# Optimization experiments

Measured on AMD Instinct MI355X. Metric: run time of the kernel, lower is better.

## Reference

```python
import math
import jax, jax.numpy as jnp
import numpy as np

K_KDE = 50
K_RIPS = 16
SCALE = 30.0
DESTNUM = 10
THRESHOLD = 1.0  # hardcoded in topograd_loss
N, D = 8192, 64


def _knn(x, k):
    """Brute-force k-NN with squared L2 distances (faiss IndexFlatL2 semantics,
    self included as nearest neighbour). Returns (sq_dists[N,k], idxs[N,k]),
    neighbours sorted by increasing distance."""
    sq = jnp.sum(x * x, axis=1)
    d = sq[:, None] + sq[None, :] - 2.0 * (x @ x.T)  # [N,N]
    neg, idx = jax.lax.top_k(-d, k)
    return -neg, idx


def _cluster(density, rips_idxs, threshold):
    """Union-find re-implementation of the numba `cluster` routine.
    Iterates points from high density (index N-1) to low; each point joins the
    entry of its highest-index upward neighbour; other upward neighbours'
    entries are merged if their persistence is below threshold, and every
    cross-entry comparison emits a persistence pair (entry_idx, ref_idx).
    Returns the raw pers_pairs array (without the [-1,-1] sentinel rows)."""
    n = density.shape[0]
    parent = np.arange(n)
    name = np.arange(n)  # name[root] = entry id (a point index)

    def find(i):
        root = i
        while parent[root] != root:
            root = parent[root]
        while parent[i] != root:  # path compression
            parent[i], i = root, parent[i]
        return root

    pairs = []
    for i in range(n - 2, -1, -1):
        nbr = rips_idxs[i]
        us = nbr[nbr > i]  # upward (denser, already-processed) neighbours
        if us.size == 0:
            continue  # point i forms its own singleton entry
        e_up = name[find(int(us.max()))]
        parent[find(i)] = find(e_up)  # append i to entry e_up
        for j in us:
            ei = name[find(int(j))]
            if ei != e_up:
                pairs.append((ei, i))
                if density[ei] - density[i] < threshold:
                    parent[find(ei)] = find(e_up)  # merge entry ei into e_up
    return np.asarray(pairs, dtype=np.int64).reshape(-1, 2)


def _pd_pairs(pairs, n):
    """For each unique entry id in pairs[:,0], keep (entry_id, max ref idx)."""
    maxref = np.full(n, -1, dtype=np.int64)
    np.maximum.at(maxref, pairs[:, 0], pairs[:, 1])
    uniq = np.unique(pairs[:, 0])
    return np.stack([uniq, maxref[uniq]], axis=1)


def setup_inputs() -> dict:
    key = jax.random.key(0)
    x = jax.random.normal(key, (N, D), dtype=jnp.float32)
    return {"x": x}


def reference(x):
    # --- KNN kernel density estimate (differentiable) ---
    vals, _ = _knn(x, K_KDE)
    res = jnp.sum(jnp.exp(-vals / SCALE), axis=1) / (K_KDE * SCALE)
    dens = res / jnp.max(res)
    # --- sort by ascending density ---
    sorted_idxs = jnp.argsort(dens)
    dens_s = dens[sorted_idxs]
    x_s = x[sorted_idxs]
    # --- delta-Rips graph on sorted points ---
    _, rips_idxs = _knn(x_s, K_RIPS)
    # --- persistence clustering (non-differentiable, host) ---
    pairs = _cluster(np.asarray(dens_s), np.asarray(rips_idxs), THRESHOLD)
    pd = jnp.asarray(_pd_pairs(pairs, x.shape[0]))  # [P,2] int64
    # --- topological loss ---
    oripd = dens_s[pd]  # [P,2] (birth, death) densities
    sidx = jnp.argsort(oripd[:, 0] - oripd[:, 1])  # ascending persistence
    changepairs = pd[sidx[:-DESTNUM]]
    nochangepairs = pd[sidx[-DESTNUM:-1]]
    dest = jax.lax.stop_gradient(oripd[sidx[-1]])  # torch.as_tensor detaches
    pd11 = dens_s[changepairs]
    weakdist = jnp.sum(pd11[:, 0] - pd11[:, 1]) / math.sqrt(2.0)
    strongdist = jnp.sum(jnp.linalg.norm(dens_s[nochangepairs] - dest, axis=1))
    return weakdist + strongdist
```

## Files before the change

### kernel.cpp

```cpp
#include <hip/hip_runtime.h>
#include <stdint.h>

#define NN 8192
#define DD 64

__global__ __launch_bounds__(256) void k_pre(const float* __restrict__ x, float* __restrict__ xT,
                                             float* __restrict__ sq, int do_tr){
  __shared__ float tile[64*65];
  const int tid = threadIdx.x;
  const int b = blockIdx.x;
  for (int k = 0; k < 4; ++k){
    const int idx4 = tid + k*256;
    const float4 v = ((const float4*)(x + (size_t)b*4096))[idx4];
    const int row = idx4 >> 4, d0 = (idx4 & 15) * 4;
    tile[row*65 + d0 + 0] = v.x;
    tile[row*65 + d0 + 1] = v.y;
    tile[row*65 + d0 + 2] = v.z;
    tile[row*65 + d0 + 3] = v.w;
  }
  __syncthreads();
  if (do_tr){
    const int jj = tid & 15;
    const int dq = tid >> 4;
    for (int k = 0; k < 4; ++k){
      const int d = dq + 16*k;
      float4 o;
      o.x = tile[(jj*4+0)*65 + d];
      o.y = tile[(jj*4+1)*65 + d];
      o.z = tile[(jj*4+2)*65 + d];
      o.w = tile[(jj*4+3)*65 + d];
      ((float4*)xT)[(size_t)d*2048 + b*16 + jj] = o;
    }
  }
  if (tid < 64){
    float acc = 0.f;
    const float* rp = tile + tid*65;
    for (int d = 0; d < 64; ++d) acc = fmaf(rp[d], rp[d], acc);
    sq[b*64 + tid] = acc;
  }
}

template<bool XT>
__device__ __forceinline__ void dists_1024(const float* __restrict__ x, const float* __restrict__ xT,
                                           const float* __restrict__ xi, int jbase, int tid,
                                           float acc[8][4]){
#pragma unroll
  for (int r = 0; r < 8; ++r)
#pragma unroll
    for (int q = 0; q < 4; ++q) acc[r][q] = 0.f;
  const int j0 = jbase + tid*4;
  for (int dq = 0; dq < 16; ++dq){
    float4 vj[4];
    if (XT){
#pragma unroll
      for (int s = 0; s < 4; ++s)
        vj[s] = ((const float4*)xT)[(size_t)(dq*4+s)*2048 + (j0 >> 2)];
    } else {
#pragma unroll
      for (int s = 0; s < 4; ++s){
        const int d = dq*4 + s;
        vj[s].x = x[(size_t)(j0+0)*64 + d];
        vj[s].y = x[(size_t)(j0+1)*64 + d];
        vj[s].z = x[(size_t)(j0+2)*64 + d];
        vj[s].w = x[(size_t)(j0+3)*64 + d];
      }
    }
#pragma unroll
    for (int r = 0; r < 8; ++r){
      const float4 wv = ((const float4*)(xi + r*64))[dq];
      acc[r][0] = fmaf(vj[0].x, wv.x, acc[r][0]);
      acc[r][1] = fmaf(vj[0].y, wv.x, acc[r][1]);
      acc[r][2] = fmaf(vj[0].z, wv.x, acc[r][2]);
      acc[r][3] = fmaf(vj[0].w, wv.x, acc[r][3]);
      acc[r][0] = fmaf(vj[1].x, wv.y, acc[r][0]);
      acc[r][1] = fmaf(vj[1].y, wv.y, acc[r][1]);
      acc[r][2] = fmaf(vj[1].z, wv.y, acc[r][2]);
      acc[r][3] = fmaf(vj[1].w, wv.y, acc[r][3]);
      acc[r][0] = fmaf(vj[2].x, wv.z, acc[r][0]);
      acc[r][1] = fmaf(vj[2].y, wv.z, acc[r][1]);
      acc[r][2] = fmaf(vj[2].z, wv.z, acc[r][2]);
      acc[r][3] = fmaf(vj[2].w, wv.z, acc[r][3]);
      acc[r][0] = fmaf(vj[3].x, wv.w, acc[r][0]);
      acc[r][1] = fmaf(vj[3].y, wv.w, acc[r][1]);
      acc[r][2] = fmaf(vj[3].z, wv.w, acc[r][2]);
      acc[r][3] = fmaf(vj[3].w, wv.w, acc[r][3]);
    }
  }
}

template<bool XT>
__global__ __launch_bounds__(256) void k_cand(const float* __restrict__ x, const float* __restrict__ xT,
                                              const float* __restrict__ sq,
                                              float* __restrict__ res, unsigned short* __restrict__ nn16){
  __shared__ float xi[8*64];
  __shared__ float sqi_s[8];
  __shared__ float tubs[8];
  __shared__ __align__(16) unsigned long long cand[8*512];
  __shared__ unsigned ccnt[8];
  float* samp = (float*)cand;
  const int tid = threadIdx.x;
  const int i0 = blockIdx.x * 8;
  for (int t = tid; t < 8*64; t += 256) xi[t] = x[(size_t)i0*64 + t];
  if (tid < 8){ sqi_s[tid] = sq[i0+tid]; ccnt[tid] = 0u; }
  __syncthreads();
  float sqir[8];
#pragma unroll
  for (int r = 0; r < 8; ++r) sqir[r] = sqi_s[r];

  const int w0 = (blockIdx.x * 1024) & 8191;
  {
    float acc[8][4];
    dists_1024<XT>(x, xT, xi, w0, tid, acc);
    float sqj[4];
#pragma unroll
    for (int q = 0; q < 4; ++q) sqj[q] = sq[w0 + tid*4 + q];
#pragma unroll
    for (int r = 0; r < 8; ++r)
#pragma unroll
      for (int q = 0; q < 4; ++q)
        samp[r*1024 + tid*4 + q] = (sqir[r] + sqj[q]) - 2.f*acc[r][q];
  }
  __syncthreads();
  {
    const int wv = tid >> 6, lane = tid & 63;
    for (int rr = 0; rr < 2; ++rr){
      const int r = wv + rr*4;
      float v[16];
#pragma unroll
      for (int k2 = 0; k2 < 16; ++k2) v[k2] = samp[r*1024 + lane + 64*k2];
      unsigned lo = 0u, hi = 0x7F800001u;
      while (hi - lo > 1u){
        const unsigned mid = (lo + hi) >> 1;
        const float pf = __uint_as_float(mid);
        int c = 0;
#pragma unroll
        for (int k2 = 0; k2 < 16; ++k2) c += (v[k2] < pf) ? 1 : 0;
#pragma unroll
        for (int off = 32; off; off >>= 1) c += __shfl_xor(c, off);
        if (c >= 32) hi = mid; else lo = mid;
      }
      if (lane == 0) tubs[r] = __uint_as_float(hi);
    }
  }
  __syncthreads();
  float tubr[8];
#pragma unroll
  for (int r = 0; r < 8; ++r) tubr[r] = tubs[r];
  for (int t = tid; t < 8*512; t += 256) cand[t] = ~0ULL;
  __syncthreads();

  for (int pass = 0; pass < 8; ++pass){
    const int jb = pass*1024;
    float acc[8][4];
    dists_1024<XT>(x, xT, xi, jb, tid, acc);
    const int j0 = jb + tid*4;
    float sqj[4];
#pragma unroll
    for (int q = 0; q < 4; ++q) sqj[q] = sq[j0 + q];
#pragma unroll
    for (int r = 0; r < 8; ++r){
#pragma unroll
      for (int q = 0; q < 4; ++q){
        const float dist = (sqir[r] + sqj[q]) - 2.f*acc[r][q];
        if (dist < tubr[r]){
          const unsigned pos = atomicAdd(&ccnt[r], 1u);
          if (pos < 512u){
            unsigned u = __float_as_uint(dist);
            u = ((int)u < 0) ? ~u : (u | 0x80000000u);
            cand[r*512 + pos] = (((unsigned long long)u) << 13) | (unsigned)(j0 + q);
          }
        }
      }
    }
  }
  __syncthreads();

  for (int k = 2; k <= 512; k <<= 1){
    for (int jj2 = k >> 1; jj2 > 0; jj2 >>= 1){
      const int mm = tid;
      const int i = ((mm & ~(jj2-1)) << 1) | (mm & (jj2-1));
      const int p = i | jj2;
      const bool up2 = ((i & k) == 0);
#pragma unroll
      for (int r = 0; r < 8; ++r){
        unsigned long long a = cand[r*512+i], bb = cand[r*512+p];
        if ((a > bb) == up2){ cand[r*512+i] = bb; cand[r*512+p] = a; }
      }
      __syncthreads();
    }
  }

  const int wv2 = tid >> 6, lane2 = tid & 63;
  for (int rr = 0; rr < 2; ++rr){
    const int r = wv2*2 + rr;
    const unsigned long long kk = cand[r*512 + lane2];
    float e = 0.f;
    if (lane2 < 50){
      unsigned u2 = (unsigned)(kk >> 13);
      u2 = (u2 & 0x80000000u) ? (u2 & 0x7FFFFFFFu) : ~u2;
      e = expf(-__uint_as_float(u2) / 30.f);
    }
#pragma unroll
    for (int off = 32; off; off >>= 1) e += __shfl_down(e, off);
    if (lane2 == 0) res[i0+r] = e / 1500.f;
    if (lane2 < 16) nn16[(size_t)(i0+r)*16 + lane2] = (unsigned short)(kk & 8191ULL);
  }
}

__device__ __forceinline__ unsigned long long shfl64_xor(unsigned long long v, int off){
  return (((unsigned long long)(unsigned)__shfl_xor((int)(v >> 32), off)) << 32)
       | (unsigned long long)(unsigned)__shfl_xor((int)(v & 0xFFFFFFFFu), off);
}

__global__ __launch_bounds__(256) void k_rank(const float* __restrict__ res,
                                              unsigned short* __restrict__ rank,
                                              float* __restrict__ dens_s){
  __shared__ __align__(16) unsigned long long keys[NN];
  __shared__ float red[256];
  __shared__ unsigned short pcnt[256];
  const int tid = threadIdx.x;
  float m = 0.f;
  for (int t = tid; t < NN; t += 256) m = fmaxf(m, res[t]);
  red[tid] = m; __syncthreads();
  for (int o = 128; o; o >>= 1){ if (tid < o) red[tid] = fmaxf(red[tid], red[tid+o]); __syncthreads(); }
  const float mr = red[0];
  __syncthreads();
  for (int t = tid; t < NN; t += 256){
    const float dnv = res[t] / mr;
    keys[t] = (((unsigned long long)__float_as_uint(dnv)) << 13) | (unsigned)t;
  }
  __syncthreads();
  const int i = blockIdx.x*128 + (tid & 127);
  const unsigned long long ki = keys[i];
  const int j0 = (tid >> 7) * (NN/2);
  int c = 0;
#pragma unroll 8
  for (int j = 0; j < NN/2; ++j) c += (keys[j0 + j] < ki) ? 1 : 0;
  pcnt[tid] = (unsigned short)c;
  __syncthreads();
  if (tid < 128){
    const int r = (int)pcnt[tid] + (int)pcnt[tid + 128];
    rank[i] = (unsigned short)r;
    dens_s[r] = __uint_as_float((unsigned)(ki >> 13));
  }
}

__global__ __launch_bounds__(256) void k_ups(const unsigned short* __restrict__ rank,
                                             const unsigned short* __restrict__ nn16,
                                             unsigned short* __restrict__ ups_t){
  __shared__ __align__(16) unsigned short rk[NN];
  const int tid = threadIdx.x;
  for (int t = tid; t < NN/8; t += 256) ((uint4*)rk)[t] = ((const uint4*)rank)[t];
  __syncthreads();
  const int o = blockIdx.x*256 + tid;
  const int p = rk[o];
  const uint4 n0 = ((const uint4*)nn16)[(size_t)o*2];
  const uint4 n1 = ((const uint4*)nn16)[(size_t)o*2 + 1];
  unsigned nw[8] = {n0.x, n0.y, n0.z, n0.w, n1.x, n1.y, n1.z, n1.w};
  unsigned short outv[16];
  int cnt = 0;
  for (int k = 0; k < 16; ++k){
    const unsigned nb = (nw[k >> 1] >> ((k & 1) * 16)) & 0xFFFFu;
    const unsigned r = rk[nb];
    if ((int)r > p){
      int q = cnt++;
      while (q > 0 && outv[q-1] < (unsigned short)r){ outv[q] = outv[q-1]; --q; }
      outv[q] = (unsigned short)r;
    }
  }
  for (int k = cnt; k < 16; ++k) outv[k] = 0;
  unsigned short* dst = ups_t + (size_t)p*16;
  uint4 a, b;
  a.x = (unsigned)outv[0] | ((unsigned)outv[1] << 16);
  a.y = (unsigned)outv[2] | ((unsigned)outv[3] << 16);
  a.z = (unsigned)outv[4] | ((unsigned)outv[5] << 16);
  a.w = (unsigned)outv[6] | ((unsigned)outv[7] << 16);
  b.x = (unsigned)outv[8] | ((unsigned)outv[9] << 16);
  b.y = (unsigned)outv[10] | ((unsigned)outv[11] << 16);
  b.z = (unsigned)outv[12] | ((unsigned)outv[13] << 16);
  b.w = (unsigned)outv[14] | ((unsigned)outv[15] << 16);
  ((uint4*)dst)[0] = a;
  ((uint4*)dst)[1] = b;
}

__device__ __forceinline__ unsigned uf_find2(volatile unsigned short* comp, unsigned x){
  unsigned r = comp[x];
  while (true){
    const unsigned g = comp[r];
    if (g == r) break;
    comp[x] = (unsigned short)g;
    x = r; r = g;
  }
  return r;
}

__global__ __launch_bounds__(1024) void k_msf(const float* __restrict__ dens_s,
                                              unsigned short* __restrict__ ups_t,
                                              unsigned long long* __restrict__ edges,
                                              int edgecap,
                                              float* __restrict__ out){
  __shared__ __align__(16) float dens[NN];
  __shared__ __align__(16) unsigned short P[NN];
  __shared__ __align__(16) unsigned short pkid[NN];
  __shared__ __align__(16) unsigned short death[NN];
  __shared__ __align__(16) unsigned short pkrank[4096];
  __shared__ __align__(16) unsigned short comp[4096];
  __shared__ __align__(16) unsigned short hook[4096];
  __shared__ __align__(16) unsigned bestv[4096];
  __shared__ __align__(16) unsigned long long msf[4096];
  __shared__ unsigned long long wred[17];
  __shared__ unsigned long long sel[10];
  __shared__ unsigned ecnt_s, ecnt2_s, mcnt_s, chg_s, flat_s, dcnt_s;
  unsigned* scan1 = (unsigned*)msf;
  float* red = (float*)msf;
  unsigned* dlist = bestv;

  const int tid = threadIdx.x;
  const int lane = tid & 63;

  for (int t = tid; t < NN/4; t += 1024)
    ((float4*)dens)[t] = ((const float4*)dens_s)[t];
  for (int t = tid; t < NN; t += 1024){
    const unsigned u0 = ups_t[(size_t)t*16];
    P[t] = (u0 == 0u) ? (unsigned short)t : (unsigned short)u0;
    death[t] = 0xFFFFu;
  }
  if (tid == 0){ ecnt_s = 0u; mcnt_s = 0u; dcnt_s = 0u; }
  __syncthreads();

  for (int rd = 0; rd < 13; ++rd){
    for (int pp = 0; pp < 8; ++pp){
      const int p = tid + pp*1024;
      const unsigned v = P[p];
      const unsigned w2 = P[v];
      if (w2 != v) P[p] = (unsigned short)w2;
    }
    __syncthreads();
  }

  {
    const int p0 = tid*8;
    int c = 0;
    for (int k = 0; k < 8; ++k) c += (P[p0+k] == (unsigned short)(p0+k)) ? 1 : 0;
    scan1[tid] = (unsigned)c; __syncthreads();
    for (int s = 1; s < 1024; s <<= 1){
      const unsigned v = scan1[tid];
      const unsigned u = (tid >= s) ? scan1[tid-s] : 0u;
      __syncthreads();
      scan1[tid] = v + u;
      __syncthreads();
    }
    int base = (int)scan1[tid] - c;
    for (int k = 0; k < 8; ++k){
      const int p = p0 + k;
      if (P[p] == (unsigned short)p){
        pkid[p] = (unsigned short)base;
        if (base < 4096) pkrank[base] = (unsigned short)p;
        ++base;
      }
    }
  }
  __syncthreads();
  int Npk = (int)scan1[1023];
  if (Npk > 4096) Npk = 4096;
  __syncthreads();

  for (int pp = 0; pp < 8; ++pp){
    const int p = tid + pp*1024;
    const uint4 a4 = ((const uint4*)ups_t)[(size_t)p*2];
    const uint4 b4 = ((const uint4*)ups_t)[(size_t)p*2 + 1];
    unsigned uu[8] = {a4.x, a4.y, a4.z, a4.w, b4.x, b4.y, b4.z, b4.w};
    unsigned edv[15];
    int nd = 0;
    const unsigned u0 = uu[0] & 0xFFFFu;
    if (u0 != 0u){
      const unsigned m0 = P[u0];
      const unsigned m0id = pkid[m0];
      for (int k = 1; k < 16; ++k){
        const unsigned uk = (uu[k >> 1] >> ((k & 1) * 16)) & 0xFFFFu;
        if (uk == 0u) break;
        const unsigned v = P[uk];
        if (v == m0) continue;
        const unsigned vid = pkid[v];
        bool dup = false;
        for (int j = 0; j < nd; ++j) dup = dup || ((edv[j] >> 16) == vid);
        if (dup) continue;
        edv[nd++] = (vid << 16) | m0id;
      }
    }
    unsigned off = (unsigned)nd;
    for (int s = 1; s < 64; s <<= 1){
      const unsigned o = (unsigned)__shfl_up((int)off, s);
      if (lane >= s) off += o;
    }
    const unsigned tot = (unsigned)__shfl((int)off, 63);
    unsigned wb = 0u;
    if (lane == 0 && tot) wb = atomicAdd(&ecnt_s, tot);
    wb = (unsigned)__shfl((int)wb, 0);
    const unsigned mybase = wb + off - (unsigned)nd;
    for (int k = 0; k < nd; ++k){
      const unsigned pos = mybase + (unsigned)k;
      if ((int)pos < edgecap)
        edges[pos] = (((unsigned long long)(unsigned)p) << 32) | (unsigned long long)edv[k];
    }
  }
  __syncthreads();
  int Ecur = ((int)ecnt_s < edgecap) ? (int)ecnt_s : edgecap;

  unsigned long long* eb_in  = edges;
  unsigned long long* eb_out = (unsigned long long*)ups_t;
  for (int t = tid; t < Npk; t += 1024) comp[t] = (unsigned short)t;
  __syncthreads();
  for (int round = 0; round < 16 && Ecur > 0; ++round){
    for (int t = tid; t < Npk; t += 1024){ bestv[t] = 0u; hook[t] = 0xFFFFu; }
    if (tid == 0){ chg_s = 0u; ecnt2_s = 0u; }
    __syncthreads();
    for (int base = 0; base < Ecur; base += 1024){
      const int e = base + tid;
      bool keep = false;
      unsigned long long ed = 0ULL;
      if (e < Ecur){
        ed = eb_in[e];
        const unsigned a = (unsigned)(ed >> 16) & 0xFFFFu;
        const unsigned b = (unsigned)ed & 0xFFFFu;
        const unsigned ra = comp[a], rb = comp[b];
        if (ra != rb){
          keep = true;
          const unsigned key = ((((unsigned)(ed >> 32)) + 1u) << 18) | (unsigned)e;
          atomicMax(&bestv[ra], key);
          atomicMax(&bestv[rb], key);
        }
      }
      const unsigned long long bal = __ballot(keep);
      const unsigned cnt = (unsigned)__popcll(bal);
      const unsigned pfx = (unsigned)__popcll(bal & ((1ULL << lane) - 1ULL));
      unsigned wb = 0u;
      if (lane == 0 && cnt) wb = atomicAdd(&ecnt2_s, cnt);
      wb = (unsigned)__shfl((int)wb, 0);
      if (keep && (wb + pfx) < 32768u) eb_out[wb + pfx] = ed;
    }
    __syncthreads();
    for (int t = tid; t < Npk; t += 1024){
      if (comp[t] == (unsigned short)t && bestv[t] != 0u){
        const unsigned long long ed = eb_in[bestv[t] & 0x3FFFFu];
        const unsigned a = (unsigned)(ed >> 16) & 0xFFFFu;
        const unsigned b = (unsigned)ed & 0xFFFFu;
        const unsigned ra = comp[a], rb = comp[b];
        hook[t] = (unsigned short)((ra == (unsigned)t) ? rb : ra);
      }
    }
    __syncthreads();
    for (int t = tid; t < Npk; t += 1024){
      const unsigned o = hook[t];
      if (o != 0xFFFFu && !(hook[o] == (unsigned short)t && (unsigned)t < o)){
        comp[t] = (unsigned short)o;
        chg_s = 1u;
        const unsigned long long ed = eb_in[bestv[t] & 0x3FFFFu];
        const unsigned pos = atomicAdd(&mcnt_s, 1u);
        if (pos < 4096u) msf[pos] = (((ed >> 32) + 1ULL) << 32) | (ed & 0xFFFFFFFFULL);
      }
    }
    __syncthreads();
    for (;;){
      if (tid == 0) flat_s = 0u;
      __syncthreads();
      for (int t = tid; t < Npk; t += 1024){
        const unsigned c = comp[t];
        const unsigned cc = comp[c];
        if (cc != c){ comp[t] = (unsigned short)cc; flat_s = 1u; }
      }
      __syncthreads();
      if (flat_s == 0u) break;
    }
    const int En = ((int)ecnt2_s < 32768) ? (int)ecnt2_s : 32767;
    const unsigned ch = chg_s;
    __syncthreads();
    Ecur = En;
    { unsigned long long* t2 = eb_in; eb_in = eb_out; eb_out = t2; }
    if (ch == 0u) break;
  }

  const int M = ((int)mcnt_s < 4096) ? (int)mcnt_s : 4095;
  int W = 64; while (W < M) W <<= 1;
  for (int t = M + tid; t < W; t += 1024) msf[t] = 0ULL;
  for (int t = tid; t < Npk; t += 1024) comp[t] = (unsigned short)t;
  __syncthreads();
  for (int k = 2; k <= W; k <<= 1){
    for (int j = k >> 1; j > 0; j >>= 1){
      for (int m2 = tid; m2 < W/2; m2 += 1024){
        const int i = ((m2 & ~(j-1)) << 1) | (m2 & (j-1));
        const int p = i | j;
        const bool up = ((i & k) == 0);
        const unsigned long long a = msf[i], b = msf[p];
        if ((a < b) == up){ msf[i] = b; msf[p] = a; }
      }
      __syncthreads();
    }
  }

  {
    const int nb = (M + 63) >> 6;
    for (int bch = 0; bch < nb; ++bch){
      if (tid < 64){
        const int ei = bch*64 + lane;
        unsigned ra = 0xFFFFu, rb = 0xFFFFu, wgt = 0u;
        if (ei < M){
          const unsigned long long e = msf[ei];
          const unsigned a = ((unsigned)e >> 16) & 0xFFFFu;
          const unsigned b = (unsigned)e & 0xFFFFu;
          wgt = (unsigned)(e >> 32) - 1u;
          ra = uf_find2(comp, a);
          rb = uf_find2(comp, b);
        }
        unsigned kra = 0xFFFFu, krb = 0xFFFFu;
        for (int i = 0; i < 64; ++i){
          const unsigned rai = (unsigned)__builtin_amdgcn_readlane((int)ra, i);
          const unsigned rbi = (unsigned)__builtin_amdgcn_readlane((int)rb, i);
          if (rai == 0xFFFFu || rai == rbi) continue;
          if (lane == i){ kra = rai; krb = rbi; }
          ra = (ra == rai) ? rbi : ra;
          rb = (rb == rai) ? rbi : rb;
        }
        if (kra != 0xFFFFu){
          death[pkrank[kra]] = (unsigned short)wgt;
          comp[kra] = (unsigned short)krb;
        }
      }
      __syncthreads();
      for (int t = tid; t < Npk; t += 1024){
        const unsigned c = comp[t];
        const unsigned cc = comp[c];
        if (cc != c) comp[t] = (unsigned short)cc;
      }
      __syncthreads();
    }
  }
  __syncthreads();

  float s = 0.f;
  for (int e = tid; e < NN; e += 1024){
    const int dr = death[e];
    if (dr != 0xFFFF) s += dens[e] - dens[dr];
  }
  red[tid] = s; __syncthreads();
  for (int o = 512; o; o >>= 1){ if (tid < o) red[tid] += red[tid+o]; __syncthreads(); }
  const float S = red[0];

  for (int e8 = 0; e8 < 8; ++e8){
    const int e = tid + e8*1024;
    const int dr = death[e];
    const bool have = (dr != 0xFFFF);
    const unsigned long long bal = __ballot(have);
    const unsigned cnt = (unsigned)__popcll(bal);
    const unsigned pfx = (unsigned)__popcll(bal & ((1ULL << lane) - 1ULL));
    unsigned wb = 0u;
    if (lane == 0 && cnt) wb = atomicAdd(&dcnt_s, cnt);
    wb = (unsigned)__shfl((int)wb, 0);
    if (have && (wb + pfx) < 4096u) dlist[wb + pfx] = ((unsigned)e << 13) | (unsigned)dr;
  }
  __syncthreads();
  const int Dm = ((int)dcnt_s < 4096) ? (int)dcnt_s : 4096;

  unsigned long long last = ~0ULL;
  for (int t10 = 0; t10 < 10; ++t10){
    unsigned long long km = 0ULL;
    for (int i = tid; i < Dm; i += 1024){
      const unsigned pk = dlist[i];
      const unsigned e = pk >> 13, dr = pk & 8191u;
      const float pers = dens[e] - dens[dr];
      const unsigned long long k = (((unsigned long long)__float_as_uint(pers)) << 13) | e;
      if (k < last && k > km) km = k;
    }
    for (int off = 32; off; off >>= 1){
      const unsigned long long o = shfl64_xor(km, off);
      km = (o > km) ? o : km;
    }
    if (lane == 0) wred[tid >> 6] = km;
    __syncthreads();
    if (tid < 64){
      unsigned long long v = (tid < 16) ? wred[tid] : 0ULL;
      for (int off = 8; off; off >>= 1){
        const unsigned long long o = shfl64_xor(v, off);
        v = (o > v) ? o : v;
      }
      if (tid == 0) wred[16] = v;
    }
    __syncthreads();
    const unsigned long long st = wred[16];
    if (tid == 0) sel[t10] = st;
    last = st;
    __syncthreads();
  }
  if (tid == 0){
    float top = 0.f;
    for (int t10 = 0; t10 < 10; ++t10)
      if (sel[t10]) top += __uint_as_float((unsigned)(sel[t10] >> 13));
    float strong = 0.f, dest0 = 0.f, dest1 = 0.f;
    if (sel[0]){
      const unsigned e0 = (unsigned)(sel[0] & 8191ULL);
      dest0 = dens[e0]; dest1 = dens[death[e0]];
    }
    for (int t10 = 1; t10 < 10; ++t10){
      if (!sel[t10]) continue;
      const unsigned e = (unsigned)(sel[t10] & 8191ULL);
      const float a = dens[e] - dest0;
      const float b = dens[death[e]] - dest1;
      strong += sqrtf(a*a + b*b);
    }
    out[0] = (S - top) / 1.41421356237309515f + strong;
  }
}

extern "C" void kernel_launch(void* const* d_in, const int* in_sizes, int n_in,
                              void* d_out, int out_size, void* d_ws, size_t ws_size,
                              hipStream_t stream){
  const float* x = (const float*)d_in[0];
  char* w = (char*)d_ws;
  float*          sq     = (float*)(w + 0);
  float*          res    = (float*)(w + 32768);
  float*          dens_s = (float*)(w + 65536);
  unsigned short* rank   = (unsigned short*)(w + 98304);
  unsigned short* nn16   = (unsigned short*)(w + 114688);
  unsigned short* ups_t  = (unsigned short*)(w + 376832);
  float*          xT     = (float*)(w + 655360);
  const int use_xt = (ws_size >= (size_t)(655360 + NN*DD*4)) ? 1 : 0;
  unsigned long long* edges = use_xt ? (unsigned long long*)(w + 655360)
                                     : (unsigned long long*)(w + 114688);
  const int edgecap = use_xt ? 262143 : 32767;

  k_pre<<<128, 256, 0, stream>>>(x, xT, sq, use_xt);
  if (use_xt) k_cand<true ><<<1024, 256, 0, stream>>>(x, xT, sq, res, nn16);
  else        k_cand<false><<<1024, 256, 0, stream>>>(x, xT, sq, res, nn16);
  k_rank<<<64, 256, 0, stream>>>(res, rank, dens_s);
  k_ups <<<32, 256, 0, stream>>>(rank, nn16, ups_t);
  k_msf <<<1, 1024, 0, stream>>>(dens_s, ups_t, edges, edgecap, (float*)d_out);
}
```

Before: 532.8 us.

## Screen kNN candidates with bf16 MFMA then rescore survivors in fp32

Adds a bf16 pre-packed fragment layout of x in k_pre and a new k_cand path that computes the full distance sweep with MFMA 16x16x32 bf16 instructions. Points that pass a loosened threshold (margin of 2.0) are collected as indices, and their exact fp32 distances are then recomputed before insertion into the candidate list. The aim is to replace the scalar fp32 FMA distance sweep, the dominant cost, with matrix-core throughput. In exchange it adds a second filtering stage and a candidate buffer capped at 1024 per row, which could overflow, and the bf16 margin may not be enough to keep every true neighbour. Half the MFMA tile rows are padding because each block handles only 8 query rows.

Result: slower. 633.3 us (+18.9%).

```diff
diff --git a/kernel.cpp b/kernel.cpp
--- a/kernel.cpp
+++ b/kernel.cpp
@@ -4,8 +4,17 @@
 #define NN 8192
 #define DD 64
 
+using bf16x8 = __attribute__((ext_vector_type(8))) short;
+using f32x4  = __attribute__((ext_vector_type(4))) float;
+
+__device__ __forceinline__ unsigned short f2bf(float f){
+  unsigned u = __float_as_uint(f);
+  return (unsigned short)((u + 0x7FFFu + ((u >> 16) & 1u)) >> 16);
+}
+
 __global__ __launch_bounds__(256) void k_pre(const float* __restrict__ x, float* __restrict__ xT,
-                                             float* __restrict__ sq, int do_tr){
+                                             float* __restrict__ sq, int do_tr,
+                                             uint4* __restrict__ xfrag, int do_frag){
   __shared__ float tile[64*65];
   const int tid = threadIdx.x;
   const int b = blockIdx.x;
@@ -30,6 +39,24 @@
       o.z = tile[(jj*4+2)*65 + d];
       o.w = tile[(jj*4+3)*65 + d];
       ((float4*)xT)[(size_t)d*2048 + b*16 + jj] = o;
+    }
+  }
+  if (do_frag){
+    for (int ch = tid; ch < 512; ch += 256){
+      const int c  = ch & 15;
+      const int q  = (ch >> 4) & 3;
+      const int m  = (ch >> 6) & 1;
+      const int gl = ch >> 7;
+      const float* sp = tile + (gl*16 + c)*65 + m*32 + q*8;
+      unsigned short h[8];
+#pragma unroll
+      for (int i2 = 0; i2 < 8; ++i2) h[i2] = f2bf(sp[i2]);
+      uint4 o;
+      o.x = (unsigned)h[0] | ((unsigned)h[1] << 16);
+      o.y = (unsigned)h[2] | ((unsigned)h[3] << 16);
+      o.z = (unsigned)h[4] | ((unsigned)h[5] << 16);
+      o.w = (unsigned)h[6] | ((unsigned)h[7] << 16);
+      xfrag[(size_t)b*512 + ch] = o;
     }
   }
   if (tid < 64){
@@ -88,20 +115,27 @@
   }
 }
 
-template<bool XT>
+template<bool XT, bool MF>
 __global__ __launch_bounds__(256) void k_cand(const float* __restrict__ x, const float* __restrict__ xT,
                                               const float* __restrict__ sq,
-                                              float* __restrict__ res, unsigned short* __restrict__ nn16){
-  __shared__ float xi[8*64];
-  __shared__ float sqi_s[8];
-  __shared__ float tubs[8];
+                                              float* __restrict__ res, unsigned short* __restrict__ nn16,
+                                              const uint4* __restrict__ xfrag){
+  __shared__ __align__(16) float xi[8*64];
+  __shared__ float sqi_s[16];
+  __shared__ float tubs[16];
   __shared__ __align__(16) unsigned long long cand[8*512];
   __shared__ unsigned ccnt[8];
+  __shared__ unsigned ccnt2[8];
+  __shared__ unsigned short candidx[MF ? 8*1024 : 16];
   float* samp = (float*)cand;
   const int tid = threadIdx.x;
   const int i0 = blockIdx.x * 8;
   for (int t = tid; t < 8*64; t += 256) xi[t] = x[(size_t)i0*64 + t];
-  if (tid < 8){ sqi_s[tid] = sq[i0+tid]; ccnt[tid] = 0u; }
+  if (tid < 16){
+    sqi_s[tid] = (tid < 8) ? sq[i0+tid] : 0.f;
+    tubs[tid] = 0.f;
+    if (tid < 8){ ccnt[tid] = 0u; ccnt2[tid] = 0u; }
+  }
   __syncthreads();
   float sqir[8];
 #pragma unroll
@@ -149,25 +183,97 @@
   for (int t = tid; t < 8*512; t += 256) cand[t] = ~0ULL;
   __syncthreads();
 
-  for (int pass = 0; pass < 8; ++pass){
-    const int jb = pass*1024;
-    float acc[8][4];
-    dists_1024<XT>(x, xT, xi, jb, tid, acc);
-    const int j0 = jb + tid*4;
-    float sqj[4];
-#pragma unroll
-    for (int q = 0; q < 4; ++q) sqj[q] = sq[j0 + q];
-#pragma unroll
+  if constexpr (MF){
+    const int l   = tid & 63;
+    const int w   = tid >> 6;
+    const int qh  = l >> 4;
+    const int c16 = l & 15;
+    bf16x8 a0, a1;
+#pragma unroll
+    for (int i2 = 0; i2 < 8; ++i2){ a0[i2] = 0; a1[i2] = 0; }
+    if (c16 < 8){
+      const float* ap = xi + c16*64 + qh*8;
+#pragma unroll
+      for (int i2 = 0; i2 < 8; ++i2){
+        a0[i2] = (short)f2bf(ap[i2]);
+        a1[i2] = (short)f2bf(ap[i2 + 32]);
+      }
+    }
+    float thr2v[4];
+#pragma unroll
+    for (int rg = 0; rg < 4; ++rg) thr2v[rg] = tubs[qh*4 + rg] + 2.0f - sqi_s[qh*4 + rg];
+
+    const bf16x8* bfp = (const bf16x8*)xfrag + (size_t)w*128 + l;
+    const float*  sqp = sq + w*16 + c16;
+    for (int it = 0; it < 128; ++it){
+      const bf16x8 b0 = bfp[(size_t)it*512];
+      const bf16x8 b1 = bfp[(size_t)it*512 + 64];
+      f32x4 acc = {0.f, 0.f, 0.f, 0.f};
+      acc = __builtin_amdgcn_mfma_f32_16x16x32_bf16(a0, b0, acc, 0, 0, 0);
+      acc = __builtin_amdgcn_mfma_f32_16x16x32_bf16(a1, b1, acc, 0, 0, 0);
+      const float sqj = sqp[it*64];
+      if (l < 32){
+        const int j = (it*4 + w)*16 + c16;
+#pragma unroll
+        for (int rg = 0; rg < 4; ++rg){
+          const float v = fmaf(-2.f, acc[rg], sqj);
+          if (v < thr2v[rg]){
+            const int r = qh*4 + rg;
+            const unsigned pos = atomicAdd(&ccnt2[r], 1u);
+            if (pos < 1024u) candidx[r*1024 + pos] = (unsigned short)j;
+          }
+        }
+      }
+    }
+    __syncthreads();
     for (int r = 0; r < 8; ++r){
-#pragma unroll
-      for (int q = 0; q < 4; ++q){
-        const float dist = (sqir[r] + sqj[q]) - 2.f*acc[r][q];
-        if (dist < tubr[r]){
+      const int cnt = ((int)ccnt2[r] < 1024) ? (int)ccnt2[r] : 1024;
+      for (int t = tid; t < cnt; t += 256){
+        const int j = candidx[r*1024 + t];
+        const float* xj = x + (size_t)j*64;
+        const float* xr = xi + r*64;
+        float acc = 0.f;
+#pragma unroll
+        for (int d4 = 0; d4 < 16; ++d4){
+          const float4 vj4 = ((const float4*)xj)[d4];
+          const float4 wi4 = ((const float4*)xr)[d4];
+          acc = fmaf(vj4.x, wi4.x, acc);
+          acc = fmaf(vj4.y, wi4.y, acc);
+          acc = fmaf(vj4.z, wi4.z, acc);
+          acc = fmaf(vj4.w, wi4.w, acc);
+        }
+        const float dist = (sqir[r] + sq[j]) - 2.f*acc;
+        if (dist < tubs[r]){
           const unsigned pos = atomicAdd(&ccnt[r], 1u);
           if (pos < 512u){
             unsigned u = __float_as_uint(dist);
             u = ((int)u < 0) ? ~u : (u | 0x80000000u);
-            cand[r*512 + pos] = (((unsigned long long)u) << 13) | (unsigned)(j0 + q);
+            cand[r*512 + pos] = (((unsigned long long)u) << 13) | (unsigned)j;
+          }
+        }
+      }
+    }
+  } else {
+    for (int pass = 0; pass < 8; ++pass){
+      const int jb = pass*1024;
+      float acc[8][4];
+      dists_1024<XT>(x, xT, xi, jb, tid, acc);
+      const int j0 = jb + tid*4;
+      float sqj[4];
+#pragma unroll
+      for (int q = 0; q < 4; ++q) sqj[q] = sq[j0 + q];
+#pragma unroll
+      for (int r = 0; r < 8; ++r){
+#pragma unroll
+        for (int q = 0; q < 4; ++q){
+          const float dist = (sqir[r] + sqj[q]) - 2.f*acc[r][q];
+          if (dist < tubr[r]){
+            const unsigned pos = atomicAdd(&ccnt[r], 1u);
+            if (pos < 512u){
+              unsigned u = __float_as_uint(dist);
+              u = ((int)u < 0) ? ~u : (u | 0x80000000u);
+              cand[r*512 + pos] = (((unsigned long long)u) << 13) | (unsigned)(j0 + q);
+            }
           }
         }
       }
@@ -623,14 +729,17 @@
   unsigned short* nn16   = (unsigned short*)(w + 114688);
   unsigned short* ups_t  = (unsigned short*)(w + 376832);
   float*          xT     = (float*)(w + 655360);
+  uint4*          xfrag  = (uint4*)(w + 655360 + (size_t)NN*DD*4);
   const int use_xt = (ws_size >= (size_t)(655360 + NN*DD*4)) ? 1 : 0;
+  const int use_mf = (ws_size >= (size_t)(655360 + NN*DD*4 + NN*DD*2)) ? 1 : 0;
   unsigned long long* edges = use_xt ? (unsigned long long*)(w + 655360)
                                      : (unsigned long long*)(w + 114688);
   const int edgecap = use_xt ? 262143 : 32767;
 
-  k_pre<<<128, 256, 0, stream>>>(x, xT, sq, use_xt);
-  if (use_xt) k_cand<true ><<<1024, 256, 0, stream>>>(x, xT, sq, res, nn16);
-  else        k_cand<false><<<1024, 256, 0, stream>>>(x, xT, sq, res, nn16);
+  k_pre<<<128, 256, 0, stream>>>(x, xT, sq, use_xt, xfrag, use_mf);
+  if (use_mf)      k_cand<true , true ><<<1024, 256, 0, stream>>>(x, xT, sq, res, nn16, xfrag);
+  else if (use_xt) k_cand<true , false><<<1024, 256, 0, stream>>>(x, xT, sq, res, nn16, xfrag);
+  else             k_cand<false, false><<<1024, 256, 0, stream>>>(x, xT, sq, res, nn16, xfrag);
   k_rank<<<64, 256, 0, stream>>>(res, rank, dens_s);
   k_ups <<<32, 256, 0, stream>>>(rank, nn16, ups_t);
   k_msf <<<1, 1024, 0, stream>>>(dens_s, ups_t, edges, edgecap, (float*)d_out);
```
